# Optimization experiments

Hardware: AMD Instinct MI355X
Metric: run time of the kernel (lower is better)

Reference implementation:

```python
import jax, jax.numpy as jnp
import numpy as np

# --- 3D Sobel kernels (smoothing [1,2,1] x derivative [-1,0,1]) ---
_H = np.array([1.0, 2.0, 1.0], np.float32)
_G = np.array([-1.0, 0.0, 1.0], np.float32)
SOBEL_X = jnp.asarray(np.einsum('i,j,k->ijk', _H, _H, _G))  # deriv along W
SOBEL_Y = jnp.asarray(np.einsum('i,j,k->ijk', _H, _G, _H))  # deriv along H
SOBEL_Z = jnp.asarray(np.einsum('i,j,k->ijk', _G, _H, _H))  # deriv along D

UPDATE_RATE = 0.25
ALIVE_THRESH = 0.1


def _depthwise3d(xp, kern3, C):
    # xp: [B,C,D+2,H+2,W+2] circular-padded; kern3: [3,3,3] shared across channels
    k = jnp.broadcast_to(kern3[None, None], (C, 1, 3, 3, 3))
    return jax.lax.conv_general_dilated(
        xp, k, window_strides=(1, 1, 1), padding='VALID',
        dimension_numbers=('NCDHW', 'OIDHW', 'NCDHW'), feature_group_count=C)


def setup_inputs() -> dict:
    key = jax.random.key(0)
    k1, k2, k3, k4, k5 = jax.random.split(key, 5)
    B, C, S = 8, 16, 64
    HID = 32
    x = jax.random.normal(k1, (B, C, S, S, S), dtype=jnp.float32)
    rand_mask = jax.random.uniform(k2, (B, C, S, S, S), dtype=jnp.float32)
    # 1x1 conv weights, init normal(std=0.001) as in the torch module
    W1 = 0.001 * jax.random.normal(k3, (HID, 4 * C), dtype=jnp.float32)
    b1 = 0.001 * jax.random.normal(k4, (HID,), dtype=jnp.float32)
    W2 = 0.001 * jax.random.normal(k5, (C, HID), dtype=jnp.float32)
    return {"x": x, "rand_mask": rand_mask, "W1": W1, "b1": b1, "W2": W2}


def reference(x, rand_mask, W1, b1, W2):
    B, C, D, H, W = x.shape
    # perception: circular pad + depthwise sobel convs, concat with identity
    xp = jnp.pad(x, ((0, 0), (0, 0), (1, 1), (1, 1), (1, 1)), mode='wrap')
    gx = _depthwise3d(xp, SOBEL_X, C)
    gy = _depthwise3d(xp, SOBEL_Y, C)
    gz = _depthwise3d(xp, SOBEL_Z, C)
    perc = jnp.concatenate([gx, gy, gz, x], axis=1)  # [B,4C,D,H,W]
    # 1x1 conv MLP
    h = jax.nn.relu(jnp.einsum('bcdhw,oc->bodhw', perc, W1)
                    + b1[None, :, None, None, None])
    dy = jnp.einsum('bcdhw,oc->bodhw', h, W2)  # [B,C,D,H,W]
    # stochastic update mask: floor(rand + rate) is 1 with prob rate
    upd = jnp.floor(rand_mask + UPDATE_RATE)
    y = x + dy * upd
    # alive mask: 3x3x3 max pool (zero... -inf pad) on alpha channel 3
    alpha = y[:, 3]  # [B,D,H,W]
    pooled = jax.lax.reduce_window(
        alpha, -jnp.inf, jax.lax.max, (1, 3, 3, 3), (1, 1, 1, 1),
        [(0, 0), (1, 1), (1, 1), (1, 1)])
    alive = (pooled > ALIVE_THRESH).astype(y.dtype)
    return y * alive[:, None]
```

## Files before the change

kernel.cpp:

```cpp
#include <hip/hip_runtime.h>
#include <hip/hip_bf16.h>
#include <math.h>

#define SD   64
#define NC   16
#define NHID 32
#define NB   8
#define ALIVE_T 0.1f
#define LSTR 160

typedef float        f32x4  __attribute__((ext_vector_type(4)));
typedef short        bf16x8 __attribute__((ext_vector_type(8)));
typedef unsigned int u32x2  __attribute__((ext_vector_type(2)));

static __device__ __forceinline__ unsigned short f2bf(float f) {
    return __builtin_bit_cast(unsigned short, __float2bfloat16(f));
}
static __device__ __forceinline__ unsigned pack2(float lo, float hi) {
    return (unsigned)f2bf(lo) | ((unsigned)f2bf(hi) << 16);
}

__global__ __launch_bounds__(256, 4) void nca_step(
    const float* __restrict__ x, const float* __restrict__ rm,
    const float* __restrict__ W1, const float* __restrict__ b1,
    const float* __restrict__ W2, float* __restrict__ y,
    float* __restrict__ alpha)
{
    const int tid  = threadIdx.x;
    const int lane = tid & 63;
    const int wid  = tid >> 6;
    const int r    = blockIdx.x * 4 + wid;
    const int h    = r & 63;
    const int d    = (r >> 6) & 63;
    const int b    = r >> 12;

    const int lg = lane >> 4;
    const int ln = lane & 15;

    __shared__ __align__(16) unsigned char lds_all[4][64 * LSTR];
    unsigned char* lds   = lds_all[wid];
    unsigned char* myrow = lds + lane * LSTR;

    bf16x8 a1[2][2];
    #pragma unroll
    for (int mt = 0; mt < 2; ++mt)
      #pragma unroll
      for (int ks = 0; ks < 2; ++ks) {
        const float* wp = W1 + (ln + 16 * mt) * 64 + ks * 32 + lg * 8;
        f32x4 w0 = *(const f32x4*)wp;
        f32x4 w1 = *(const f32x4*)(wp + 4);
        bf16x8 f;
        f[0]=(short)f2bf(w0[0]); f[1]=(short)f2bf(w0[1]);
        f[2]=(short)f2bf(w0[2]); f[3]=(short)f2bf(w0[3]);
        f[4]=(short)f2bf(w1[0]); f[5]=(short)f2bf(w1[1]);
        f[6]=(short)f2bf(w1[2]); f[7]=(short)f2bf(w1[3]);
        a1[mt][ks] = f;
      }
    bf16x8 a2;
    {
        const float* wp = W2 + ln * 32 + lg * 8;
        f32x4 w0 = *(const f32x4*)wp;
        f32x4 w1 = *(const f32x4*)(wp + 4);
        a2[0]=(short)f2bf(w0[0]); a2[1]=(short)f2bf(w0[1]);
        a2[2]=(short)f2bf(w0[2]); a2[3]=(short)f2bf(w0[3]);
        a2[4]=(short)f2bf(w1[0]); a2[5]=(short)f2bf(w1[1]);
        a2[6]=(short)f2bf(w1[2]); a2[7]=(short)f2bf(w1[3]);
    }
    const f32x4 b1lo = *(const f32x4*)(b1 + lg * 4);
    const f32x4 b1hi = *(const f32x4*)(b1 + 16 + lg * 4);

    const int dm = (d + 63) & 63, dp = (d + 1) & 63;
    const int hm = (h + 63) & 63, hp = (h + 1) & 63;
    const int lm = (lane + 63) & 63, lp = (lane + 1) & 63;

    const int o_mm = (dm << 12) + (hm << 6) + lane;
    const int o_m0 = (dm << 12) + (h  << 6) + lane;
    const int o_mp = (dm << 12) + (hp << 6) + lane;
    const int o_0m = (d  << 12) + (hm << 6) + lane;
    const int o_00 = (d  << 12) + (h  << 6) + lane;
    const int o_0p = (d  << 12) + (hp << 6) + lane;
    const int o_pm = (dp << 12) + (hm << 6) + lane;
    const int o_p0 = (dp << 12) + (h  << 6) + lane;
    const int o_pp = (dp << 12) + (hp << 6) + lane;

    float xv[NC];

    #pragma unroll
    for (int c0 = 0; c0 < NC; c0 += 2) {
        float fa[4], fb[4];
        #pragma unroll
        for (int cc = 0; cc < 2; ++cc) {
            const int c = c0 + cc;
            const float* base = x + (((size_t)(b * NC + c)) << 18);
            float v_mm = base[o_mm], v_m0 = base[o_m0], v_mp = base[o_mp];
            float v_0m = base[o_0m], v_00 = base[o_00], v_0p = base[o_0p];
            float v_pm = base[o_pm], v_p0 = base[o_p0], v_pp = base[o_pp];
            float am = v_mm + 2.f * v_m0 + v_mp;
            float a0 = v_0m + 2.f * v_00 + v_0p;
            float ap = v_pm + 2.f * v_p0 + v_pp;
            float gm = v_mp - v_mm;
            float g0 = v_0p - v_0m;
            float gp = v_pp - v_pm;
            float P_hh = am + 2.f * a0 + ap;
            float P_hg = gm + 2.f * g0 + gp;
            float P_gh = ap - am;
            float gx = __shfl(P_hh, lp, 64) - __shfl(P_hh, lm, 64);
            float gy = __shfl(P_hg, lm, 64) + 2.f * P_hg + __shfl(P_hg, lp, 64);
            float gz = __shfl(P_gh, lm, 64) + 2.f * P_gh + __shfl(P_gh, lp, 64);
            float* o = cc ? fb : fa;
            o[0] = gx; o[1] = gy; o[2] = gz; o[3] = v_00;
            xv[c] = v_00;
        }
        *(unsigned*)(myrow +       2 * c0) = pack2(fa[0], fb[0]);
        *(unsigned*)(myrow + 32 +  2 * c0) = pack2(fa[1], fb[1]);
        *(unsigned*)(myrow + 64 +  2 * c0) = pack2(fa[2], fb[2]);
        *(unsigned*)(myrow + 96 +  2 * c0) = pack2(fa[3], fb[3]);
    }

    f32x4 acc1[2][4];
    #pragma unroll
    for (int nt = 0; nt < 4; ++nt) { acc1[0][nt] = b1lo; acc1[1][nt] = b1hi; }

    #pragma unroll
    for (int ks = 0; ks < 2; ++ks) {
        bf16x8 bp[4];
        #pragma unroll
        for (int nt = 0; nt < 4; ++nt)
            bp[nt] = *(const bf16x8*)(lds + (ln + 16 * nt) * LSTR + ks * 64 + lg * 16);
        #pragma unroll
        for (int mt = 0; mt < 2; ++mt)
          #pragma unroll
          for (int nt = 0; nt < 4; ++nt)
            acc1[mt][nt] = __builtin_amdgcn_mfma_f32_16x16x32_bf16(
                a1[mt][ks], bp[nt], acc1[mt][nt], 0, 0, 0);
    }

    #pragma unroll
    for (int mt = 0; mt < 2; ++mt)
      #pragma unroll
      for (int nt = 0; nt < 4; ++nt) {
        f32x4 v = acc1[mt][nt];
        u32x2 u;
        u[0] = pack2(fmaxf(v[0], 0.f), fmaxf(v[1], 0.f));
        u[1] = pack2(fmaxf(v[2], 0.f), fmaxf(v[3], 0.f));
        *(u32x2*)(lds + (ln + 16 * nt) * LSTR + (lg * 8 + 32 * mt)) = u;
      }

    f32x4 acc2[4];
    #pragma unroll
    for (int nt = 0; nt < 4; ++nt) acc2[nt] = (f32x4){0.f, 0.f, 0.f, 0.f};
    #pragma unroll
    for (int nt = 0; nt < 4; ++nt) {
        bf16x8 bh = *(const bf16x8*)(lds + (ln + 16 * nt) * LSTR + lg * 16);
        acc2[nt] = __builtin_amdgcn_mfma_f32_16x16x32_bf16(a2, bh, acc2[nt], 0, 0, 0);
    }

    #pragma unroll
    for (int nt = 0; nt < 4; ++nt)
        *(f32x4*)(lds + (ln + 16 * nt) * LSTR + 64 + lg * 16) = acc2[nt];

    float dyv[NC];
    #pragma unroll
    for (int j = 0; j < 4; ++j) {
        f32x4 t = *(const f32x4*)(myrow + 64 + j * 16);
        dyv[4 * j + 0] = t[0]; dyv[4 * j + 1] = t[1];
        dyv[4 * j + 2] = t[2]; dyv[4 * j + 3] = t[3];
    }

    const size_t voff = ((size_t)d << 12) + ((size_t)h << 6) + lane;
    #pragma unroll
    for (int ch = 0; ch < NC; ++ch) {
        const size_t idx = (((size_t)(b * NC + ch)) << 18) + voff;
        float upd = floorf(rm[idx] + 0.25f);
        float yv  = fmaf(dyv[ch], upd, xv[ch]);
        y[idx] = yv;
        if (ch == 3) alpha[(((size_t)b) << 18) + voff] = yv;
    }
}

__global__ __launch_bounds__(256, 4) void alive_mask(
    const float* __restrict__ alpha, float* __restrict__ y)
{
    const int tid  = blockIdx.x * 256 + threadIdx.x;
    const int lane = threadIdx.x & 63;
    const int wq   = tid & 15;
    const int w4   = wq << 2;
    const int h    = (tid >> 4) & 63;
    const int d    = (tid >> 10) & 63;
    const int b    = tid >> 16;

    const float* ab = alpha + (((size_t)b) << 18);

    float m0 = -INFINITY, m1 = -INFINITY, m2 = -INFINITY, m3 = -INFINITY;
    #pragma unroll
    for (int dz = -1; dz <= 1; ++dz) {
        int dd = d + dz;
        if (dd < 0 || dd > 63) continue;
        #pragma unroll
        for (int hy = -1; hy <= 1; ++hy) {
            int hh = h + hy;
            if (hh < 0 || hh > 63) continue;
            const float4 v = *reinterpret_cast<const float4*>(
                ab + (dd << 12) + (hh << 6) + w4);
            m0 = fmaxf(m0, v.x); m1 = fmaxf(m1, v.y);
            m2 = fmaxf(m2, v.z); m3 = fmaxf(m3, v.w);
        }
    }
    float left  = __shfl(m3, (lane + 63) & 63, 64);
    float right = __shfl(m0, (lane + 1) & 63, 64);
    if (wq == 0)  left  = -INFINITY;
    if (wq == 15) right = -INFINITY;

    float p0 = fmaxf(left, fmaxf(m0, m1));
    float p1 = fmaxf(m0,   fmaxf(m1, m2));
    float p2 = fmaxf(m1,   fmaxf(m2, m3));
    float p3 = fmaxf(m2,   fmaxf(m3, right));

    const bool d0 = !(p0 > ALIVE_T);
    const bool d1 = !(p1 > ALIVE_T);
    const bool d2 = !(p2 > ALIVE_T);
    const bool d3 = !(p3 > ALIVE_T);

    if (d0 | d1 | d2 | d3) {
        const size_t voff = ((size_t)d << 12) + ((size_t)h << 6) + w4;
        #pragma unroll
        for (int ch = 0; ch < NC; ++ch) {
            float* p = y + (((size_t)(b * NC + ch)) << 18) + voff;
            if (d0) p[0] = 0.f;
            if (d1) p[1] = 0.f;
            if (d2) p[2] = 0.f;
            if (d3) p[3] = 0.f;
        }
    }
}

extern "C" void kernel_launch(void* const* d_in, const int* in_sizes, int n_in,
                              void* d_out, int out_size, void* d_ws, size_t ws_size,
                              hipStream_t stream) {
    const float* x  = (const float*)d_in[0];
    const float* rm = (const float*)d_in[1];
    const float* W1 = (const float*)d_in[2];
    const float* b1 = (const float*)d_in[3];
    const float* W2 = (const float*)d_in[4];
    float* y     = (float*)d_out;
    float* alpha = (float*)d_ws;

    const int rows    = NB * SD * SD;
    const int blocks1 = rows / 4;
    const int blocks2 = (NB * SD * SD * 16) / 256;

    nca_step<<<blocks1, 256, 0, stream>>>(x, rm, W1, b1, W2, y, alpha);
    alive_mask<<<blocks2, 256, 0, stream>>>(alpha, y);
}
```

Baseline: 370.2 us.

## Swizzle LDS tile and interleave perception features for 128-byte rows

Replaces the padded 160-byte LDS row stride with a 128-byte row and an XOR swizzle on 16-byte chunks, aiming to avoid bank conflicts without padding. Perception features are now interleaved per channel pair (gx,gy,gz,x for two channels), so each lane writes one 16-byte vector store instead of four scalar stores. W1 loads are permuted to match the new K ordering, weight loading and conversion are moved after the stencil phase to cut live registers, and the bias add moves from the accumulator init to the ReLU epilogue. The W1 gather becomes eight scalar strided loads, which adds global load instructions.

```diff
diff --git a/kernel.cpp b/kernel.cpp
--- a/kernel.cpp
+++ b/kernel.cpp
@@ -7,7 +7,7 @@
 #define NHID 32
 #define NB   8
 #define ALIVE_T 0.1f
-#define LSTR 160
+#define LROW 128
 
 typedef float        f32x4  __attribute__((ext_vector_type(4)));
 typedef short        bf16x8 __attribute__((ext_vector_type(8)));
@@ -18,6 +18,10 @@
 }
 static __device__ __forceinline__ unsigned pack2(float lo, float hi) {
     return (unsigned)f2bf(lo) | ((unsigned)f2bf(hi) << 16);
+}
+static __device__ __forceinline__ unsigned char* swz(
+    unsigned char* lds, int r0, int c, int o) {
+    return lds + r0 * LROW + (((c ^ (r0 & 7)) << 4) + o);
 }
 
 __global__ __launch_bounds__(256, 4) void nca_step(
@@ -37,37 +41,8 @@
     const int lg = lane >> 4;
     const int ln = lane & 15;
 
-    __shared__ __align__(16) unsigned char lds_all[4][64 * LSTR];
-    unsigned char* lds   = lds_all[wid];
-    unsigned char* myrow = lds + lane * LSTR;
-
-    bf16x8 a1[2][2];
-    #pragma unroll
-    for (int mt = 0; mt < 2; ++mt)
-      #pragma unroll
-      for (int ks = 0; ks < 2; ++ks) {
-        const float* wp = W1 + (ln + 16 * mt) * 64 + ks * 32 + lg * 8;
-        f32x4 w0 = *(const f32x4*)wp;
-        f32x4 w1 = *(const f32x4*)(wp + 4);
-        bf16x8 f;
-        f[0]=(short)f2bf(w0[0]); f[1]=(short)f2bf(w0[1]);
-        f[2]=(short)f2bf(w0[2]); f[3]=(short)f2bf(w0[3]);
-        f[4]=(short)f2bf(w1[0]); f[5]=(short)f2bf(w1[1]);
-        f[6]=(short)f2bf(w1[2]); f[7]=(short)f2bf(w1[3]);
-        a1[mt][ks] = f;
-      }
-    bf16x8 a2;
-    {
-        const float* wp = W2 + ln * 32 + lg * 8;
-        f32x4 w0 = *(const f32x4*)wp;
-        f32x4 w1 = *(const f32x4*)(wp + 4);
-        a2[0]=(short)f2bf(w0[0]); a2[1]=(short)f2bf(w0[1]);
-        a2[2]=(short)f2bf(w0[2]); a2[3]=(short)f2bf(w0[3]);
-        a2[4]=(short)f2bf(w1[0]); a2[5]=(short)f2bf(w1[1]);
-        a2[6]=(short)f2bf(w1[2]); a2[7]=(short)f2bf(w1[3]);
-    }
-    const f32x4 b1lo = *(const f32x4*)(b1 + lg * 4);
-    const f32x4 b1hi = *(const f32x4*)(b1 + 16 + lg * 4);
+    __shared__ __align__(16) unsigned char lds_all[4][64 * LROW];
+    unsigned char* lds = lds_all[wid];
 
     const int dm = (d + 63) & 63, dp = (d + 1) & 63;
     const int hm = (h + 63) & 63, hp = (h + 1) & 63;
@@ -87,11 +62,9 @@
 
     #pragma unroll
     for (int c0 = 0; c0 < NC; c0 += 2) {
-        float fa[4], fb[4];
-        #pragma unroll
-        for (int cc = 0; cc < 2; ++cc) {
-            const int c = c0 + cc;
-            const float* base = x + (((size_t)(b * NC + c)) << 18);
+        float gxa, gya, gza, xa, gxb, gyb, gzb, xb;
+        {
+            const float* base = x + (((size_t)(b * NC + c0)) << 18);
             float v_mm = base[o_mm], v_m0 = base[o_m0], v_mp = base[o_mp];
             float v_0m = base[o_0m], v_00 = base[o_00], v_0p = base[o_0p];
             float v_pm = base[o_pm], v_p0 = base[o_p0], v_pp = base[o_pp];
@@ -104,65 +77,98 @@
             float P_hh = am + 2.f * a0 + ap;
             float P_hg = gm + 2.f * g0 + gp;
             float P_gh = ap - am;
-            float gx = __shfl(P_hh, lp, 64) - __shfl(P_hh, lm, 64);
-            float gy = __shfl(P_hg, lm, 64) + 2.f * P_hg + __shfl(P_hg, lp, 64);
-            float gz = __shfl(P_gh, lm, 64) + 2.f * P_gh + __shfl(P_gh, lp, 64);
-            float* o = cc ? fb : fa;
-            o[0] = gx; o[1] = gy; o[2] = gz; o[3] = v_00;
-            xv[c] = v_00;
-        }
-        *(unsigned*)(myrow +       2 * c0) = pack2(fa[0], fb[0]);
-        *(unsigned*)(myrow + 32 +  2 * c0) = pack2(fa[1], fb[1]);
-        *(unsigned*)(myrow + 64 +  2 * c0) = pack2(fa[2], fb[2]);
-        *(unsigned*)(myrow + 96 +  2 * c0) = pack2(fa[3], fb[3]);
-    }
+            gxa = __shfl(P_hh, lp, 64) - __shfl(P_hh, lm, 64);
+            gya = __shfl(P_hg, lm, 64) + 2.f * P_hg + __shfl(P_hg, lp, 64);
+            gza = __shfl(P_gh, lm, 64) + 2.f * P_gh + __shfl(P_gh, lp, 64);
+            xa  = v_00;
+        }
+        {
+            const float* base = x + (((size_t)(b * NC + c0 + 1)) << 18);
+            float v_mm = base[o_mm], v_m0 = base[o_m0], v_mp = base[o_mp];
+            float v_0m = base[o_0m], v_00 = base[o_00], v_0p = base[o_0p];
+            float v_pm = base[o_pm], v_p0 = base[o_p0], v_pp = base[o_pp];
+            float am = v_mm + 2.f * v_m0 + v_mp;
+            float a0 = v_0m + 2.f * v_00 + v_0p;
+            float ap = v_pm + 2.f * v_p0 + v_pp;
+            float gm = v_mp - v_mm;
+            float g0 = v_0p - v_0m;
+            float gp = v_pp - v_pm;
+            float P_hh = am + 2.f * a0 + ap;
+            float P_hg = gm + 2.f * g0 + gp;
+            float P_gh = ap - am;
+            gxb = __shfl(P_hh, lp, 64) - __shfl(P_hh, lm, 64);
+            gyb = __shfl(P_hg, lm, 64) + 2.f * P_hg + __shfl(P_hg, lp, 64);
+            gzb = __shfl(P_gh, lm, 64) + 2.f * P_gh + __shfl(P_gh, lp, 64);
+            xb  = v_00;
+        }
+        xv[c0] = xa; xv[c0 + 1] = xb;
+        bf16x8 pk;
+        pk[0] = (short)f2bf(gxa); pk[1] = (short)f2bf(gya);
+        pk[2] = (short)f2bf(gza); pk[3] = (short)f2bf(xa);
+        pk[4] = (short)f2bf(gxb); pk[5] = (short)f2bf(gyb);
+        pk[6] = (short)f2bf(gzb); pk[7] = (short)f2bf(xb);
+        *(bf16x8*)swz(lds, lane, c0 >> 1, 0) = pk;
+    }
+
+    bf16x8 a1[2][2];
+    #pragma unroll
+    for (int mt = 0; mt < 2; ++mt)
+      #pragma unroll
+      for (int ks = 0; ks < 2; ++ks) {
+        const float* wr = W1 + (ln + 16 * mt) * 64 + ks * 8 + lg * 2;
+        bf16x8 f;
+        #pragma unroll
+        for (int j = 0; j < 8; ++j)
+            f[j] = (short)f2bf(wr[(j & 3) * 16 + (j >> 2)]);
+        a1[mt][ks] = f;
+      }
 
     f32x4 acc1[2][4];
     #pragma unroll
-    for (int nt = 0; nt < 4; ++nt) { acc1[0][nt] = b1lo; acc1[1][nt] = b1hi; }
-
-    #pragma unroll
-    for (int ks = 0; ks < 2; ++ks) {
-        bf16x8 bp[4];
-        #pragma unroll
-        for (int nt = 0; nt < 4; ++nt)
-            bp[nt] = *(const bf16x8*)(lds + (ln + 16 * nt) * LSTR + ks * 64 + lg * 16);
-        #pragma unroll
-        for (int mt = 0; mt < 2; ++mt)
-          #pragma unroll
-          for (int nt = 0; nt < 4; ++nt)
-            acc1[mt][nt] = __builtin_amdgcn_mfma_f32_16x16x32_bf16(
-                a1[mt][ks], bp[nt], acc1[mt][nt], 0, 0, 0);
-    }
-
+    for (int nt = 0; nt < 4; ++nt) {
+        acc1[0][nt] = (f32x4){0.f, 0.f, 0.f, 0.f};
+        acc1[1][nt] = (f32x4){0.f, 0.f, 0.f, 0.f};
+    }
+    #pragma unroll
+    for (int nt = 0; nt < 4; ++nt) {
+        bf16x8 bp0 = *(const bf16x8*)swz(lds, ln + 16 * nt, lg,     0);
+        bf16x8 bp1 = *(const bf16x8*)swz(lds, ln + 16 * nt, 4 + lg, 0);
+        acc1[0][nt] = __builtin_amdgcn_mfma_f32_16x16x32_bf16(a1[0][0], bp0, acc1[0][nt], 0, 0, 0);
+        acc1[1][nt] = __builtin_amdgcn_mfma_f32_16x16x32_bf16(a1[1][0], bp0, acc1[1][nt], 0, 0, 0);
+        acc1[0][nt] = __builtin_amdgcn_mfma_f32_16x16x32_bf16(a1[0][1], bp1, acc1[0][nt], 0, 0, 0);
+        acc1[1][nt] = __builtin_amdgcn_mfma_f32_16x16x32_bf16(a1[1][1], bp1, acc1[1][nt], 0, 0, 0);
+    }
+
+    const f32x4 bl = *(const f32x4*)(b1 + lg * 4);
+    const f32x4 bh = *(const f32x4*)(b1 + 16 + lg * 4);
     #pragma unroll
     for (int mt = 0; mt < 2; ++mt)
       #pragma unroll
       for (int nt = 0; nt < 4; ++nt) {
         f32x4 v = acc1[mt][nt];
+        f32x4 bb = mt ? bh : bl;
         u32x2 u;
-        u[0] = pack2(fmaxf(v[0], 0.f), fmaxf(v[1], 0.f));
-        u[1] = pack2(fmaxf(v[2], 0.f), fmaxf(v[3], 0.f));
-        *(u32x2*)(lds + (ln + 16 * nt) * LSTR + (lg * 8 + 32 * mt)) = u;
+        u[0] = pack2(fmaxf(v[0] + bb[0], 0.f), fmaxf(v[1] + bb[1], 0.f));
+        u[1] = pack2(fmaxf(v[2] + bb[2], 0.f), fmaxf(v[3] + bb[3], 0.f));
+        *(u32x2*)swz(lds, ln + 16 * nt, 2 * mt + (lg >> 1), (lg & 1) * 8) = u;
       }
 
-    f32x4 acc2[4];
-    #pragma unroll
-    for (int nt = 0; nt < 4; ++nt) acc2[nt] = (f32x4){0.f, 0.f, 0.f, 0.f};
+    bf16x8 a2;
+    #pragma unroll
+    for (int j = 0; j < 8; ++j)
+        a2[j] = (short)f2bf(W2[ln * 32 + lg * 8 + j]);
     #pragma unroll
     for (int nt = 0; nt < 4; ++nt) {
-        bf16x8 bh = *(const bf16x8*)(lds + (ln + 16 * nt) * LSTR + lg * 16);
-        acc2[nt] = __builtin_amdgcn_mfma_f32_16x16x32_bf16(a2, bh, acc2[nt], 0, 0, 0);
-    }
-
-    #pragma unroll
-    for (int nt = 0; nt < 4; ++nt)
-        *(f32x4*)(lds + (ln + 16 * nt) * LSTR + 64 + lg * 16) = acc2[nt];
+        bf16x8 bhf = *(const bf16x8*)swz(lds, ln + 16 * nt, lg, 0);
+        f32x4 acc2 = (f32x4){0.f, 0.f, 0.f, 0.f};
+        acc2 = __builtin_amdgcn_mfma_f32_16x16x32_bf16(a2, bhf, acc2, 0, 0, 0);
+        *(f32x4*)swz(lds, ln + 16 * nt, 4 + lg, 0) = acc2;
+    }
 
     float dyv[NC];
     #pragma unroll
     for (int j = 0; j < 4; ++j) {
-        f32x4 t = *(const f32x4*)(myrow + 64 + j * 16);
+        f32x4 t = *(const f32x4*)swz(lds, lane, 4 + j, 0);
         dyv[4 * j + 0] = t[0]; dyv[4 * j + 1] = t[1];
         dyv[4 * j + 2] = t[2]; dyv[4 * j + 3] = t[3];
     }
```

Measured after the change: 385.5 us. +4.1%, slower.
